# Kernel optimization log

Measured on AMD Instinct MI355X. Metric: run time of the kernel, lower is better.

## Reference

```python
import jax, jax.numpy as jnp
import numpy as np

B, T, D = 4, 2048, 2048
H, HD = 16, 128          # heads, head_dim (H*HD == D)
I = 5632                 # intermediate size
CAP = 0.25
K = int(T * CAP)         # 512 tokens selected per batch row
S = B * K                # packed sequence length
THETA = 10000.0
EPS = 1e-6


def setup_inputs() -> dict:
    key = jax.random.key(0)
    ks = jax.random.split(key, 12)
    s = 0.02
    w = lambda k, shp: jax.random.normal(k, shp, jnp.float32) * s
    return {
        "hidden_states": jax.random.normal(ks[0], (B, T, D), jnp.float32),
        "router_w": w(ks[1], (D,)),
        "router_b": jnp.zeros((1,), jnp.float32),
        "ln1_w": jnp.ones((D,), jnp.float32),
        "ln2_w": jnp.ones((D,), jnp.float32),
        "wq": w(ks[2], (D, D)), "bq": jnp.zeros((D,), jnp.float32),
        "wk": w(ks[3], (D, D)), "bk": jnp.zeros((D,), jnp.float32),
        "wv": w(ks[4], (D, D)), "bv": jnp.zeros((D,), jnp.float32),
        "wo": w(ks[5], (D, D)),
        "w_gate": w(ks[6], (D, I)),
        "w_up": w(ks[7], (D, I)),
        "w_down": w(ks[8], (I, D)),
    }


def _rms(x, w):
    return x * jax.lax.rsqrt(jnp.mean(x * x, axis=-1, keepdims=True) + EPS) * w


def _rotate_half(x):
    x1, x2 = jnp.split(x, 2, axis=-1)
    return jnp.concatenate([-x2, x1], axis=-1)


def reference(hidden_states, router_w, router_b, ln1_w, ln2_w,
              wq, bq, wk, bk, wv, bv, wo, w_gate, w_up, w_down):
    # ---- router: per-token scalar scores, top-k per batch row ----
    scores = hidden_states @ router_w + router_b[0]          # [B,T]
    _, idx = jax.lax.top_k(scores, K)                        # [B,K]
    idx = jnp.sort(idx, axis=-1)                             # causal order in packed seq

    # ---- gather selected tokens into packed batch-1 sequence ----
    sel = jnp.take_along_axis(hidden_states, idx[..., None], axis=1)  # [B,K,D]
    sel_scores = jnp.take_along_axis(scores, idx, axis=1)             # [B,K]
    x = sel.reshape(S, D)
    pos = idx.reshape(S)                                     # original token positions

    # ---- rotary tables gathered at original positions ----
    inv_freq = 1.0 / (THETA ** (jnp.arange(0, HD, 2, dtype=jnp.float32) / HD))
    freqs = pos.astype(jnp.float32)[:, None] * inv_freq[None, :]      # [S,HD/2]
    emb = jnp.concatenate([freqs, freqs], axis=-1)                    # [S,HD]
    cos, sin = jnp.cos(emb)[:, None, :], jnp.sin(emb)[:, None, :]     # [S,1,HD]

    # ---- Qwen2 decoder block (attention) ----
    h = _rms(x, ln1_w)
    q = (h @ wq + bq).reshape(S, H, HD)
    k = (h @ wk + bk).reshape(S, H, HD)
    v = (h @ wv + bv).reshape(S, H, HD)
    q = q * cos + _rotate_half(q) * sin
    k = k * cos + _rotate_half(k) * sin

    att = jnp.einsum("shd,thd->hst", q, k) / np.sqrt(HD).astype(np.float32)
    causal = jnp.tril(jnp.ones((S, S), bool))
    att = jnp.where(causal[None], att, jnp.finfo(att.dtype).min)
    p = jax.nn.softmax(att, axis=-1)
    attn_out = jnp.einsum("hst,thd->shd", p, v).reshape(S, D) @ wo
    x1 = x + attn_out

    # ---- Qwen2 decoder block (SwiGLU MLP) ----
    h2 = _rms(x1, ln2_w)
    mlp = (jax.nn.silu(h2 @ w_gate) * (h2 @ w_up)) @ w_down
    processed = x1 + mlp                                     # [S,D]

    # ---- sigmoid gate blend + scatter back ----
    gate = jax.nn.sigmoid(sel_scores).reshape(S, 1)
    blended = gate * processed + (1.0 - gate) * x            # [S,D]
    out = hidden_states.at[jnp.arange(B)[:, None], idx].set(blended.reshape(B, K, D))
    return out
```

## Files before the change

kernel.cpp:

```cpp
#include <hip/hip_runtime.h>
#include <stdint.h>

#define B_ 4
#define T_ 2048
#define D_ 2048
#define H_ 16
#define HD_ 128
#define I_ 5632
#define K_ 512
#define S_ 2048
#define D3_ (3 * D_)

typedef float f32x4 __attribute__((ext_vector_type(4)));
typedef short s16x8 __attribute__((ext_vector_type(8)));
typedef __bf16 bf16x8 __attribute__((ext_vector_type(8)));

template <typename V>
__device__ __forceinline__ auto mfma_try(V a, V b, f32x4 c, int)
    -> decltype(__builtin_amdgcn_mfma_f32_16x16x32_bf16(a, b, c, 0, 0, 0)) {
  return __builtin_amdgcn_mfma_f32_16x16x32_bf16(a, b, c, 0, 0, 0);
}
template <typename V>
__device__ __forceinline__ f32x4 mfma_try(V a, V b, f32x4 c, long) {
  return __builtin_amdgcn_mfma_f32_16x16x32_bf16(
      __builtin_bit_cast(bf16x8, a), __builtin_bit_cast(bf16x8, b), c, 0, 0, 0);
}
__device__ __forceinline__ f32x4 mfma_bf16(s16x8 a, s16x8 b, f32x4 c) {
  return mfma_try(a, b, c, 0);
}

__device__ __forceinline__ void gl_lds16(const void* g, void* l) {
  __builtin_amdgcn_global_load_lds((const __attribute__((address_space(1))) void*)g,
                                   (__attribute__((address_space(3))) void*)l, 16, 0, 0);
}

__device__ __forceinline__ unsigned short f2bf(float f) {
  unsigned u = __float_as_uint(f);
  u += 0x7FFFu + ((u >> 16) & 1);
  return (unsigned short)(u >> 16);
}
__device__ __forceinline__ float bf2f(unsigned short s) {
  return __uint_as_float(((unsigned)s) << 16);
}

__global__ __launch_bounds__(256) void k_copy_scores(const float4* __restrict__ hid,
                                                     float4* __restrict__ dst,
                                                     const float4* __restrict__ rw,
                                                     const float* __restrict__ rb,
                                                     float* __restrict__ scores) {
  int row = blockIdx.x, t = threadIdx.x;
  const float4* hr = hid + (size_t)row * (D_ / 4);
  float4* dr = dst + (size_t)row * (D_ / 4);
  float acc = 0.f;
#pragma unroll
  for (int i = 0; i < 2; i++) {
    float4 v = hr[t + i * 256];
    dr[t + i * 256] = v;
    float4 w = rw[t + i * 256];
    acc += v.x * w.x + v.y * w.y + v.z * w.z + v.w * w.w;
  }
#pragma unroll
  for (int d = 32; d; d >>= 1) acc += __shfl_xor(acc, d);
  __shared__ float red[4];
  if ((t & 63) == 0) red[t >> 6] = acc;
  __syncthreads();
  if (t == 0) scores[row] = red[0] + red[1] + red[2] + red[3] + rb[0];
}

__global__ __launch_bounds__(1024) void k_topk(const float* __restrict__ scores,
                                               int* __restrict__ pos) {
  __shared__ unsigned long long keys[T_];
  __shared__ int sidx[K_];
  int b = blockIdx.x, t = threadIdx.x;
  for (int i = t; i < T_; i += 1024) {
    unsigned u = __float_as_uint(scores[b * T_ + i]);
    u = (u & 0x80000000u) ? ~u : (u | 0x80000000u);
    keys[i] = ((unsigned long long)u << 32) | (unsigned)(~(unsigned)i);
  }
  __syncthreads();
  for (int k = 2; k <= T_; k <<= 1)
    for (int j = k >> 1; j > 0; j >>= 1) {
      for (int i = t; i < T_; i += 1024) {
        int l = i ^ j;
        if (l > i) {
          unsigned long long a = keys[i], c = keys[l];
          bool desc = ((i & k) == 0);
          if (desc ? (a < c) : (a > c)) { keys[i] = c; keys[l] = a; }
        }
      }
      __syncthreads();
    }
  if (t < K_) sidx[t] = (int)(~(unsigned)(keys[t] & 0xFFFFFFFFull));
  __syncthreads();
  for (int k = 2; k <= K_; k <<= 1)
    for (int j = k >> 1; j > 0; j >>= 1) {
      if (t < K_) {
        int i = t, l = i ^ j;
        if (l > i && l < K_) {
          int a = sidx[i], c = sidx[l];
          bool asc = ((i & k) == 0);
          if (asc ? (a > c) : (a < c)) { sidx[i] = c; sidx[l] = a; }
        }
      }
      __syncthreads();
    }
  if (t < K_) pos[b * K_ + t] = sidx[t];
}

__global__ __launch_bounds__(256) void k_gather(const float* __restrict__ hidden,
    const int* __restrict__ pos, const float* __restrict__ scores,
    const float* __restrict__ ln1w, float* __restrict__ x,
    unsigned short* __restrict__ xn, float* __restrict__ gate,
    float* __restrict__ cosb, float* __restrict__ sinb) {
  int s = blockIdx.x, t = threadIdx.x;
  int b = s >> 9, p = pos[s];
  const float* src = hidden + ((size_t)b * T_ + p) * D_;
  float v[8];
  float ss = 0.f;
#pragma unroll
  for (int i = 0; i < 8; i++) { v[i] = src[t + i * 256]; ss += v[i] * v[i]; }
  __shared__ float red[4];
#pragma unroll
  for (int d = 32; d; d >>= 1) ss += __shfl_xor(ss, d);
  if ((t & 63) == 0) red[t >> 6] = ss;
  __syncthreads();
  ss = red[0] + red[1] + red[2] + red[3];
  float scale = rsqrtf(ss / (float)D_ + 1e-6f);
  float* xd = x + (size_t)s * D_;
  unsigned short* xnd = xn + (size_t)s * D_;
#pragma unroll
  for (int i = 0; i < 8; i++) {
    int c = t + i * 256;
    xd[c] = v[i];
    xnd[c] = f2bf(v[i] * scale * ln1w[c]);
  }
  if (t == 0) gate[s] = 1.f / (1.f + expf(-scores[b * T_ + p]));
  if (t < 64) {
    float invf = powf(10000.0f, -(float)t / 64.0f);
    float f = (float)p * invf;
    cosb[s * 64 + t] = cosf(f);
    sinb[s * 64 + t] = sinf(f);
  }
}

__global__ __launch_bounds__(256) void k_transpose(const float* __restrict__ src,
                                                   unsigned short* __restrict__ dst,
                                                   int R, int C) {
  __shared__ float tile[32][33];
  int tx = threadIdx.x & 31, ty = threadIdx.x >> 5;
  int c0 = blockIdx.x * 32, r0 = blockIdx.y * 32;
#pragma unroll
  for (int i = 0; i < 4; i++) {
    int r = ty + i * 8;
    tile[r][tx] = src[(size_t)(r0 + r) * C + c0 + tx];
  }
  __syncthreads();
#pragma unroll
  for (int i = 0; i < 4; i++) {
    int r = ty + i * 8;
    dst[(size_t)(c0 + r) * R + r0 + tx] = f2bf(tile[tx][r]);
  }
}

#define SWZ(row) ((((row) >> 1) & 3) << 4)

__device__ __forceinline__ void stage16k(const unsigned short* __restrict__ g, int ldK,
                                         int row0, int k0, char* lds, int tid) {
#pragma unroll
  for (int c = 0; c < 2; c++) {
    int off = c * 8192 + tid * 16;
    int row = off >> 6;
    int cb = (off & 63) ^ SWZ(row);
    gl_lds16(g + (size_t)(row0 + row) * ldK + k0 + (cb >> 1), lds + off);
  }
}
__device__ __forceinline__ void stage8k(const unsigned short* __restrict__ g, int ldK,
                                        int row0, int k0, char* lds, int tid) {
  int off = tid * 16;
  int row = off >> 6;
  int cb = (off & 63) ^ SWZ(row);
  gl_lds16(g + (size_t)(row0 + row) * ldK + k0 + (cb >> 1), lds + off);
}
__device__ __forceinline__ void stage64r(const unsigned short* __restrict__ g, int ldK,
                                         int row0, int k0, char* lds, int tid) {
  int off = tid * 16;
  int row = off >> 6;
  int cb = (off & 63) ^ SWZ(row);
  gl_lds16(g + (size_t)(row0 + row) * ldK + k0 + (cb >> 1), lds + off);
}
__device__ __forceinline__ void stage128r(const unsigned short* __restrict__ g, int ldK,
                                          int row0, int k0, char* lds, int tid) {
#pragma unroll
  for (int c = 0; c < 2; c++) {
    int off = c * 4096 + tid * 16;
    int row = off >> 6;
    int cb = (off & 63) ^ SWZ(row);
    gl_lds16(g + (size_t)(row0 + row) * ldK + k0 + (cb >> 1), lds + off);
  }
}
__device__ __forceinline__ s16x8 ldfrag(const char* base, int row, int g) {
  return *(const s16x8*)(base + row * 64 + ((g * 16) ^ SWZ(row)));
}

__global__ __launch_bounds__(512, 2) void k_gemm_qkv8(const unsigned short* __restrict__ A,
    const unsigned short* __restrict__ Bt, unsigned short* __restrict__ C,
    const float* __restrict__ bq, const float* __restrict__ bk,
    const float* __restrict__ bv) {
  alignas(16) __shared__ short As[2][256 * 32];
  alignas(16) __shared__ short Bs[2][128 * 32];
  int tid = threadIdx.x;
  int lane = tid & 63, g = lane >> 4, lr = lane & 15;
  int wid = tid >> 6, wm = wid >> 1, wn = wid & 1;
  int m0 = blockIdx.x * 256, n0 = blockIdx.y * 128;
  f32x4 zero4 = {0.f, 0.f, 0.f, 0.f};
  f32x4 acc[4][4];
#pragma unroll
  for (int m = 0; m < 4; m++)
#pragma unroll
    for (int n = 0; n < 4; n++) acc[m][n] = zero4;
  const int nkt = D_ / 32;
  stage16k(A, D_, m0, 0, (char*)As[0], tid);
  stage8k(Bt, D_, n0, 0, (char*)Bs[0], tid);
  stage16k(A, D_, m0, 32, (char*)As[1], tid);
  stage8k(Bt, D_, n0, 32, (char*)Bs[1], tid);
  int arow = wm * 64 + lr;
  int brow = wn * 64 + lr;
  for (int t = 0; t < nkt; t++) {
    int b = t & 1;
    const char* Ab = (const char*)As[b];
    const char* Bb = (const char*)Bs[b];
    if (t + 1 < nkt) asm volatile("s_waitcnt vmcnt(3)" ::: "memory");
    else             asm volatile("s_waitcnt vmcnt(0)" ::: "memory");
    __builtin_amdgcn_s_barrier();
    s16x8 af[4], bf4[4];
#pragma unroll
    for (int i = 0; i < 4; i++) af[i] = ldfrag(Ab, arow + i * 16, g);
#pragma unroll
    for (int i = 0; i < 4; i++) bf4[i] = ldfrag(Bb, brow + i * 16, g);
    asm volatile("s_waitcnt lgkmcnt(0)" ::: "memory");
    __builtin_amdgcn_s_barrier();
    if (t + 2 < nkt) {
      stage16k(A, D_, m0, (t + 2) * 32, (char*)As[b], tid);
      stage8k(Bt, D_, n0, (t + 2) * 32, (char*)Bs[b], tid);
    }
    __builtin_amdgcn_s_setprio(1);
#pragma unroll
    for (int m = 0; m < 4; m++)
#pragma unroll
      for (int n = 0; n < 4; n++) acc[m][n] = mfma_bf16(af[m], bf4[n], acc[m][n]);
    __builtin_amdgcn_s_setprio(0);
  }
#pragma unroll
  for (int m = 0; m < 4; m++)
#pragma unroll
    for (int n = 0; n < 4; n++)
#pragma unroll
      for (int r = 0; r < 4; r++) {
        int row = m0 + wm * 64 + m * 16 + (g << 2) + r;
        int col = n0 + wn * 64 + n * 16 + lr;
        float bias = (col < D_) ? bq[col] : ((col < 2 * D_) ? bk[col - D_] : bv[col - 2 * D_]);
        C[(size_t)row * D3_ + col] = f2bf(acc[m][n][r] + bias);
      }
}

__global__ __launch_bounds__(512, 2) void k_gemm_gup8(const unsigned short* __restrict__ A,
    const unsigned short* __restrict__ Bg, const unsigned short* __restrict__ Bu,
    unsigned short* __restrict__ act) {
  alignas(16) __shared__ short As[2][256 * 32];
  alignas(16) __shared__ short Bgs[2][128 * 32];
  alignas(16) __shared__ short Bus[2][128 * 32];
  int tid = threadIdx.x;
  int lane = tid & 63, g = lane >> 4, lr = lane & 15;
  int wid = tid >> 6, wm = wid >> 1, wn = wid & 1;
  int m0 = blockIdx.x * 256, n0 = blockIdx.y * 128;
  f32x4 zero4 = {0.f, 0.f, 0.f, 0.f};
  f32x4 ag[4][4], au[4][4];
#pragma unroll
  for (int m = 0; m < 4; m++)
#pragma unroll
    for (int n = 0; n < 4; n++) { ag[m][n] = zero4; au[m][n] = zero4; }
  const int nkt = D_ / 32;
  stage16k(A, D_, m0, 0, (char*)As[0], tid);
  stage8k(Bg, D_, n0, 0, (char*)Bgs[0], tid);
  stage8k(Bu, D_, n0, 0, (char*)Bus[0], tid);
  stage16k(A, D_, m0, 32, (char*)As[1], tid);
  stage8k(Bg, D_, n0, 32, (char*)Bgs[1], tid);
  stage8k(Bu, D_, n0, 32, (char*)Bus[1], tid);
  int arow = wm * 64 + lr;
  int brow = wn * 64 + lr;
  for (int t = 0; t < nkt; t++) {
    int b = t & 1;
    const char* Ab = (const char*)As[b];
    const char* Bgb = (const char*)Bgs[b];
    const char* Bub = (const char*)Bus[b];
    if (t + 1 < nkt) asm volatile("s_waitcnt vmcnt(4)" ::: "memory");
    else             asm volatile("s_waitcnt vmcnt(0)" ::: "memory");
    __builtin_amdgcn_s_barrier();
    s16x8 af[4], bg4[4], bu4[4];
#pragma unroll
    for (int i = 0; i < 4; i++) af[i] = ldfrag(Ab, arow + i * 16, g);
#pragma unroll
    for (int i = 0; i < 4; i++) bg4[i] = ldfrag(Bgb, brow + i * 16, g);
#pragma unroll
    for (int i = 0; i < 4; i++) bu4[i] = ldfrag(Bub, brow + i * 16, g);
    asm volatile("s_waitcnt lgkmcnt(0)" ::: "memory");
    __builtin_amdgcn_s_barrier();
    if (t + 2 < nkt) {
      stage16k(A, D_, m0, (t + 2) * 32, (char*)As[b], tid);
      stage8k(Bg, D_, n0, (t + 2) * 32, (char*)Bgs[b], tid);
      stage8k(Bu, D_, n0, (t + 2) * 32, (char*)Bus[b], tid);
    }
    __builtin_amdgcn_s_setprio(1);
#pragma unroll
    for (int m = 0; m < 4; m++)
#pragma unroll
      for (int n = 0; n < 4; n++) {
        ag[m][n] = mfma_bf16(af[m], bg4[n], ag[m][n]);
        au[m][n] = mfma_bf16(af[m], bu4[n], au[m][n]);
      }
    __builtin_amdgcn_s_setprio(0);
  }
#pragma unroll
  for (int m = 0; m < 4; m++)
#pragma unroll
    for (int n = 0; n < 4; n++)
#pragma unroll
      for (int r = 0; r < 4; r++) {
        int row = m0 + wm * 64 + m * 16 + (g << 2) + r;
        int col = n0 + wn * 64 + n * 16 + lr;
        float gv = ag[m][n][r], uv = au[m][n][r];
        float si = gv / (1.f + __expf(-gv));
        act[(size_t)row * I_ + col] = f2bf(si * uv);
      }
}

__global__ __launch_bounds__(256, 2) void k_gemm_wo64(const unsigned short* __restrict__ A,
    const unsigned short* __restrict__ Bt, const float* __restrict__ xres,
    float* __restrict__ x1) {
  alignas(16) __shared__ short As[2][64 * 32];
  alignas(16) __shared__ short Bs[2][128 * 32];
  int tid = threadIdx.x;
  int lane = tid & 63, g = lane >> 4, lr = lane & 15, wid = tid >> 6;
  int m0 = blockIdx.x * 64, n0 = blockIdx.y * 128;
  f32x4 zero4 = {0.f, 0.f, 0.f, 0.f};
  f32x4 acc[4][2];
#pragma unroll
  for (int m = 0; m < 4; m++)
#pragma unroll
    for (int n = 0; n < 2; n++) acc[m][n] = zero4;
  const int nkt = D_ / 32;
  stage64r(A, D_, m0, 0, (char*)As[0], tid);
  stage128r(Bt, D_, n0, 0, (char*)Bs[0], tid);
  stage64r(A, D_, m0, 32, (char*)As[1], tid);
  stage128r(Bt, D_, n0, 32, (char*)Bs[1], tid);
  for (int t = 0; t < nkt; t++) {
    int b = t & 1;
    const char* Ab = (const char*)As[b];
    const char* Bb = (const char*)Bs[b];
    if (t + 1 < nkt) asm volatile("s_waitcnt vmcnt(3)" ::: "memory");
    else             asm volatile("s_waitcnt vmcnt(0)" ::: "memory");
    __builtin_amdgcn_s_barrier();
    s16x8 af[4], bf2[2];
#pragma unroll
    for (int i = 0; i < 4; i++) af[i] = ldfrag(Ab, i * 16 + lr, g);
#pragma unroll
    for (int j = 0; j < 2; j++) bf2[j] = ldfrag(Bb, wid * 32 + j * 16 + lr, g);
    asm volatile("s_waitcnt lgkmcnt(0)" ::: "memory");
    __builtin_amdgcn_s_barrier();
    if (t + 2 < nkt) {
      stage64r(A, D_, m0, (t + 2) * 32, (char*)As[b], tid);
      stage128r(Bt, D_, n0, (t + 2) * 32, (char*)Bs[b], tid);
    }
    __builtin_amdgcn_s_setprio(1);
#pragma unroll
    for (int m = 0; m < 4; m++)
#pragma unroll
      for (int n = 0; n < 2; n++) acc[m][n] = mfma_bf16(af[m], bf2[n], acc[m][n]);
    __builtin_amdgcn_s_setprio(0);
  }
#pragma unroll
  for (int m = 0; m < 4; m++)
#pragma unroll
    for (int n = 0; n < 2; n++)
#pragma unroll
      for (int r = 0; r < 4; r++) {
        int row = m0 + m * 16 + (g << 2) + r;
        int col = n0 + wid * 32 + n * 16 + lr;
        x1[(size_t)row * D_ + col] = acc[m][n][r] + xres[(size_t)row * D_ + col];
      }
}

__global__ __launch_bounds__(256, 2) void k_gemm_down64(const unsigned short* __restrict__ A,
    const unsigned short* __restrict__ Bt, const float* __restrict__ x1,
    const float* __restrict__ x, const float* __restrict__ gate,
    const int* __restrict__ pos, float* __restrict__ out) {
  alignas(16) __shared__ short As[2][64 * 32];
  alignas(16) __shared__ short Bs[2][128 * 32];
  int tid = threadIdx.x;
  int lane = tid & 63, g = lane >> 4, lr = lane & 15, wid = tid >> 6;
  int m0 = blockIdx.x * 64, n0 = blockIdx.y * 128;
  f32x4 zero4 = {0.f, 0.f, 0.f, 0.f};
  f32x4 acc[4][2];
#pragma unroll
  for (int m = 0; m < 4; m++)
#pragma unroll
    for (int n = 0; n < 2; n++) acc[m][n] = zero4;
  const int nkt = I_ / 32;
  stage64r(A, I_, m0, 0, (char*)As[0], tid);
  stage128r(Bt, I_, n0, 0, (char*)Bs[0], tid);
  stage64r(A, I_, m0, 32, (char*)As[1], tid);
  stage128r(Bt, I_, n0, 32, (char*)Bs[1], tid);
  for (int t = 0; t < nkt; t++) {
    int b = t & 1;
    const char* Ab = (const char*)As[b];
    const char* Bb = (const char*)Bs[b];
    if (t + 1 < nkt) asm volatile("s_waitcnt vmcnt(3)" ::: "memory");
    else             asm volatile("s_waitcnt vmcnt(0)" ::: "memory");
    __builtin_amdgcn_s_barrier();
    s16x8 af[4], bf2[2];
#pragma unroll
    for (int i = 0; i < 4; i++) af[i] = ldfrag(Ab, i * 16 + lr, g);
#pragma unroll
    for (int j = 0; j < 2; j++) bf2[j] = ldfrag(Bb, wid * 32 + j * 16 + lr, g);
    asm volatile("s_waitcnt lgkmcnt(0)" ::: "memory");
    __builtin_amdgcn_s_barrier();
    if (t + 2 < nkt) {
      stage64r(A, I_, m0, (t + 2) * 32, (char*)As[b], tid);
      stage128r(Bt, I_, n0, (t + 2) * 32, (char*)Bs[b], tid);
    }
    __builtin_amdgcn_s_setprio(1);
#pragma unroll
    for (int m = 0; m < 4; m++)
#pragma unroll
      for (int n = 0; n < 2; n++) acc[m][n] = mfma_bf16(af[m], bf2[n], acc[m][n]);
    __builtin_amdgcn_s_setprio(0);
  }
#pragma unroll
  for (int m = 0; m < 4; m++)
#pragma unroll
    for (int n = 0; n < 2; n++)
#pragma unroll
      for (int r = 0; r < 4; r++) {
        int srow = m0 + m * 16 + (g << 2) + r;
        int col = n0 + wid * 32 + n * 16 + lr;
        float proc = acc[m][n][r] + x1[(size_t)srow * D_ + col];
        float gt = gate[srow];
        float xv = x[(size_t)srow * D_ + col];
        int bb = srow >> 9;
        int p = pos[srow];
        out[((size_t)bb * T_ + p) * D_ + col] = gt * proc + (1.f - gt) * xv;
      }
}

__global__ __launch_bounds__(256) void k_rope(const unsigned short* __restrict__ qkv,
    const float* __restrict__ cosb, const float* __restrict__ sinb,
    unsigned short* __restrict__ qh, unsigned short* __restrict__ kh,
    unsigned short* __restrict__ vT) {
  int s0 = blockIdx.x * 64;
  int h = blockIdx.y;
  int t = threadIdx.x;
#pragma unroll
  for (int i = 0; i < 16; i++) {
    int flat = t + i * 256;
    int r = flat >> 6, dp = flat & 63;
    int s = s0 + r;
    float c = cosb[s * 64 + dp], sn = sinb[s * 64 + dp];
    const unsigned short* qrow = qkv + (size_t)s * D3_ + h * HD_;
    float q1 = bf2f(qrow[dp]), q2 = bf2f(qrow[dp + 64]);
    unsigned short* qdst = qh + ((size_t)h * S_ + s) * HD_;
    qdst[dp] = f2bf(q1 * c - q2 * sn);
    qdst[dp + 64] = f2bf(q2 * c + q1 * sn);
    const unsigned short* krow = qrow + D_;
    float k1 = bf2f(krow[dp]), k2 = bf2f(krow[dp + 64]);
    unsigned short* kdst = kh + ((size_t)h * S_ + s) * HD_;
    kdst[dp] = f2bf(k1 * c - k2 * sn);
    kdst[dp + 64] = f2bf(k2 * c + k1 * sn);
  }
  __shared__ unsigned short vt[128][66];
#pragma unroll
  for (int i = 0; i < 32; i++) {
    int flat = t + i * 256;
    int r = flat >> 7, d = flat & 127;
    vt[d][r] = qkv[(size_t)(s0 + r) * D3_ + 2 * D_ + h * HD_ + d];
  }
  __syncthreads();
#pragma unroll
  for (int i = 0; i < 32; i++) {
    int flat = t + i * 256;
    int d = flat >> 6, sc = flat & 63;
    vT[((size_t)h * HD_ + d) * S_ + s0 + sc] = vt[d][sc];
  }
}

__device__ __forceinline__ void stage_kv(const unsigned short* __restrict__ kh,
                                         const unsigned short* __restrict__ vT,
                                         size_t hbase, int kt, char* KsB, char* VsB, int tid) {
#pragma unroll
  for (int c = 0; c < 4; c++) {
    int off = c * 4096 + tid * 16;
    int row = off >> 8;
    int cb = (off & 255) ^ ((row & 7) << 4);
    gl_lds16(kh + hbase + (size_t)(kt * 64 + row) * HD_ + (cb >> 1), KsB + off);
  }
#pragma unroll
  for (int c = 0; c < 4; c++) {
    int off = c * 4096 + tid * 16;
    int row = off >> 7;
    int cb = (off & 127) ^ ((row & 7) << 4);
    gl_lds16(vT + hbase + (size_t)row * S_ + kt * 64 + (cb >> 1), VsB + off);
  }
}

__global__ __launch_bounds__(256, 2) void k_attn(const unsigned short* __restrict__ qh,
                                                 const unsigned short* __restrict__ kh,
                                                 const unsigned short* __restrict__ vT,
                                                 unsigned short* __restrict__ ao) {
  alignas(16) __shared__ short Ks[2][64 * 128];
  alignas(16) __shared__ short Vs[2][128 * 64];
  alignas(16) __shared__ short Ps[4][16 * 64];
  int bidx = blockIdx.x;
  int head = bidx & 15;
  int slot = bidx >> 4;
  int qt = (slot < 16) ? (31 - slot) : (slot - 16);
  int q0 = qt * 64;
  int tid = threadIdx.x, w = tid >> 6, lane = tid & 63, g = lane >> 4, lr = lane & 15;
  size_t hbase = (size_t)head * S_ * HD_;
  int qw = q0 + w * 16;
  char* PsW = (char*)&Ps[w][0];
  s16x8 qf[4];
#pragma unroll
  for (int ks = 0; ks < 4; ks++)
    qf[ks] = *(const s16x8*)&qh[hbase + (size_t)(qw + lr) * HD_ + ks * 32 + g * 8];
  f32x4 o[8];
  f32x4 zero4 = {0.f, 0.f, 0.f, 0.f};
#pragma unroll
  for (int nf = 0; nf < 8; nf++) o[nf] = zero4;
  float m_i[4], l_i[4];
#pragma unroll
  for (int r = 0; r < 4; r++) { m_i[r] = -1e30f; l_i[r] = 0.f; }
  const float sc = 0.08838834764831843f;

  stage_kv(kh, vT, hbase, 0, (char*)Ks[0], (char*)Vs[0], tid);
  if (qt > 0) stage_kv(kh, vT, hbase, 1, (char*)Ks[1], (char*)Vs[1], tid);

  for (int kt = 0; kt <= qt; kt++) {
    int b = kt & 1;
    const char* KsB = (const char*)Ks[b];
    const char* VsB = (const char*)Vs[b];
    if (kt < qt) asm volatile("s_waitcnt vmcnt(8)" ::: "memory");
    else         asm volatile("s_waitcnt vmcnt(0)" ::: "memory");
    __builtin_amdgcn_s_barrier();
    f32x4 sacc[4];
#pragma unroll
    for (int nf = 0; nf < 4; nf++) sacc[nf] = zero4;
#pragma unroll
    for (int ks = 0; ks < 4; ks++) {
      s16x8 kf[4];
#pragma unroll
      for (int nf = 0; nf < 4; nf++) {
        int row = nf * 16 + lr;
        kf[nf] = *(const s16x8*)(KsB + row * 256 + (((ks << 6) + (g << 4)) ^ ((row & 7) << 4)));
      }
#pragma unroll
      for (int nf = 0; nf < 4; nf++) sacc[nf] = mfma_bf16(qf[ks], kf[nf], sacc[nf]);
    }
    bool diag = (kt == qt);
#pragma unroll
    for (int r = 0; r < 4; r++) {
      int prow = (g << 2) + r;
      int qrow = qw + prow;
      float pv[4];
      float mx = -1e30f;
#pragma unroll
      for (int nf = 0; nf < 4; nf++) {
        float vv = sacc[nf][r] * sc;
        if (diag) {
          int kc = kt * 64 + nf * 16 + lr;
          vv = (kc <= qrow) ? vv : -1e30f;
        }
        pv[nf] = vv;
        mx = fmaxf(mx, vv);
      }
#pragma unroll
      for (int d = 1; d < 16; d <<= 1) mx = fmaxf(mx, __shfl_xor(mx, d));
      float mold = m_i[r], mnew = fmaxf(mold, mx);
      float corr = __expf(mold - mnew);
      float ssum = 0.f;
#pragma unroll
      for (int nf = 0; nf < 4; nf++) {
        float pe = __expf(pv[nf] - mnew);
        int cb = ((nf * 16 + lr) << 1) ^ ((prow & 7) << 4);
        *(unsigned short*)(PsW + prow * 128 + cb) = f2bf(pe);
        ssum += pe;
      }
#pragma unroll
      for (int d = 1; d < 16; d <<= 1) ssum += __shfl_xor(ssum, d);
      l_i[r] = l_i[r] * corr + ssum;
      m_i[r] = mnew;
#pragma unroll
      for (int nf = 0; nf < 8; nf++) o[nf][r] *= corr;
    }
    s16x8 pa[2];
#pragma unroll
    for (int ks = 0; ks < 2; ks++)
      pa[ks] = *(const s16x8*)(PsW + lr * 128 + (((ks << 6) + (g << 4)) ^ ((lr & 7) << 4)));
#pragma unroll
    for (int nf = 0; nf < 8; nf++) {
#pragma unroll
      for (int ks = 0; ks < 2; ks++) {
        int row = nf * 16 + lr;
        s16x8 vb = *(const s16x8*)(VsB + row * 128 + (((ks << 6) + (g << 4)) ^ ((row & 7) << 4)));
        o[nf] = mfma_bf16(pa[ks], vb, o[nf]);
      }
    }
    asm volatile("s_waitcnt lgkmcnt(0)" ::: "memory");
    __builtin_amdgcn_s_barrier();
    if (kt + 2 <= qt)
      stage_kv(kh, vT, hbase, kt + 2, (char*)Ks[b], (char*)Vs[b], tid);
  }
#pragma unroll
  for (int nf = 0; nf < 8; nf++)
#pragma unroll
    for (int r = 0; r < 4; r++) {
      int row = qw + (g << 2) + r;
      int col = head * HD_ + nf * 16 + lr;
      ao[(size_t)row * D_ + col] = f2bf(o[nf][r] / l_i[r]);
    }
}

__global__ __launch_bounds__(256) void k_rms2(const float* __restrict__ x1,
                                              const float* __restrict__ ln2w,
                                              unsigned short* __restrict__ xn2) {
  int s = blockIdx.x, t = threadIdx.x;
  const float* src = x1 + (size_t)s * D_;
  float v[8];
  float ss = 0.f;
#pragma unroll
  for (int i = 0; i < 8; i++) { v[i] = src[t + i * 256]; ss += v[i] * v[i]; }
  __shared__ float red[4];
#pragma unroll
  for (int d = 32; d; d >>= 1) ss += __shfl_xor(ss, d);
  if ((t & 63) == 0) red[t >> 6] = ss;
  __syncthreads();
  ss = red[0] + red[1] + red[2] + red[3];
  float scale = rsqrtf(ss / (float)D_ + 1e-6f);
  unsigned short* dst = xn2 + (size_t)s * D_;
#pragma unroll
  for (int i = 0; i < 8; i++) {
    int c = t + i * 256;
    dst[c] = f2bf(v[i] * scale * ln2w[c]);
  }
}

extern "C" void kernel_launch(void* const* d_in, const int* in_sizes, int n_in,
                              void* d_out, int out_size, void* d_ws, size_t ws_size,
                              hipStream_t stream) {
  (void)in_sizes; (void)n_in; (void)out_size; (void)ws_size;
  const float* hidden = (const float*)d_in[0];
  const float* router_w = (const float*)d_in[1];
  const float* router_b = (const float*)d_in[2];
  const float* ln1w = (const float*)d_in[3];
  const float* ln2w = (const float*)d_in[4];
  const float* wq = (const float*)d_in[5];
  const float* bq = (const float*)d_in[6];
  const float* wk = (const float*)d_in[7];
  const float* bk = (const float*)d_in[8];
  const float* wv = (const float*)d_in[9];
  const float* bv = (const float*)d_in[10];
  const float* wo = (const float*)d_in[11];
  const float* wg = (const float*)d_in[12];
  const float* wu = (const float*)d_in[13];
  const float* wd = (const float*)d_in[14];
  float* out = (float*)d_out;

  char* ws = (char*)d_ws;
  size_t off = 0;
  auto alloc = [&](size_t bytes) {
    char* p = ws + off;
    off += (bytes + 255) & ~(size_t)255;
    return p;
  };
  unsigned short* wqkvT = (unsigned short*)alloc(3ull * D_ * D_ * 2);
  unsigned short* woT = (unsigned short*)alloc((size_t)D_ * D_ * 2);
  unsigned short* wgT = (unsigned short*)alloc((size_t)I_ * D_ * 2);
  unsigned short* wuT = (unsigned short*)alloc((size_t)I_ * D_ * 2);
  unsigned short* wdT = (unsigned short*)alloc((size_t)D_ * I_ * 2);
  float* scores = (float*)alloc((size_t)B_ * T_ * 4);
  int* pos = (int*)alloc((size_t)S_ * 4);
  float* gate = (float*)alloc((size_t)S_ * 4);
  float* x = (float*)alloc((size_t)S_ * D_ * 4);
  float* x1 = (float*)alloc((size_t)S_ * D_ * 4);
  unsigned short* xn = (unsigned short*)alloc((size_t)S_ * D_ * 2);
  float* cosb = (float*)alloc((size_t)S_ * 64 * 4);
  float* sinb = (float*)alloc((size_t)S_ * 64 * 4);
  unsigned short* qkv = (unsigned short*)alloc((size_t)S_ * D3_ * 2);
  unsigned short* qh = (unsigned short*)alloc((size_t)H_ * S_ * HD_ * 2);
  unsigned short* kh = (unsigned short*)alloc((size_t)H_ * S_ * HD_ * 2);
  unsigned short* vT = (unsigned short*)alloc((size_t)H_ * S_ * HD_ * 2);
  unsigned short* ao = (unsigned short*)alloc((size_t)S_ * D_ * 2);

  k_copy_scores<<<B_ * T_, 256, 0, stream>>>((const float4*)hidden, (float4*)out,
                                             (const float4*)router_w, router_b, scores);

  k_transpose<<<dim3(D_ / 32, D_ / 32), 256, 0, stream>>>(wq, wqkvT, D_, D_);
  k_transpose<<<dim3(D_ / 32, D_ / 32), 256, 0, stream>>>(wk, wqkvT + (size_t)D_ * D_, D_, D_);
  k_transpose<<<dim3(D_ / 32, D_ / 32), 256, 0, stream>>>(wv, wqkvT + 2ull * D_ * D_, D_, D_);
  k_transpose<<<dim3(D_ / 32, D_ / 32), 256, 0, stream>>>(wo, woT, D_, D_);
  k_transpose<<<dim3(I_ / 32, D_ / 32), 256, 0, stream>>>(wg, wgT, D_, I_);
  k_transpose<<<dim3(I_ / 32, D_ / 32), 256, 0, stream>>>(wu, wuT, D_, I_);
  k_transpose<<<dim3(D_ / 32, I_ / 32), 256, 0, stream>>>(wd, wdT, I_, D_);

  k_topk<<<B_, 1024, 0, stream>>>(scores, pos);
  k_gather<<<S_, 256, 0, stream>>>(hidden, pos, scores, ln1w, x, xn, gate, cosb, sinb);

  k_gemm_qkv8<<<dim3(S_ / 256, D3_ / 128), 512, 0, stream>>>(xn, wqkvT, qkv, bq, bk, bv);
  k_rope<<<dim3(S_ / 64, H_), 256, 0, stream>>>(qkv, cosb, sinb, qh, kh, vT);
  k_attn<<<32 * H_, 256, 0, stream>>>(qh, kh, vT, ao);
  k_gemm_wo64<<<dim3(S_ / 64, D_ / 128), 256, 0, stream>>>(ao, woT, x, x1);
  k_rms2<<<S_, 256, 0, stream>>>(x1, ln2w, xn);
  k_gemm_gup8<<<dim3(S_ / 256, I_ / 128), 512, 0, stream>>>(xn, wgT, wuT, qkv);
  k_gemm_down64<<<dim3(S_ / 64, D_ / 128), 256, 0, stream>>>(qkv, wdT, x1, x, gate, pos, out);
}
```

Measured before the change: 566.9 us.

## Triple-buffer LDS in GEMM kernels to drop one barrier per k-step

Moves the QKV, Wo and down-projection GEMMs from double to triple LDS buffering. Each k-step now needs one barrier instead of two, and the LDS fragment reads overlap the prefetch issued for step t+2. The transpose kernel also writes four bf16 values per thread as a single vector store. The cost is 50% more shared memory per block, which may lower occupancy, notably for the 512-thread QKV kernel with launch bounds of 2 blocks.

Result: slower. 583.4 us (+2.9%).

```diff
diff --git a/kernel.cpp b/kernel.cpp
--- a/kernel.cpp
+++ b/kernel.cpp
@@ -155,11 +155,14 @@
     tile[r][tx] = src[(size_t)(r0 + r) * C + c0 + tx];
   }
   __syncthreads();
-#pragma unroll
-  for (int i = 0; i < 4; i++) {
-    int r = ty + i * 8;
-    dst[(size_t)(c0 + r) * R + r0 + tx] = f2bf(tile[tx][r]);
-  }
+  int drow = threadIdx.x >> 3;
+  int dc4 = (threadIdx.x & 7) * 4;
+  ushort4 v;
+  v.x = f2bf(tile[dc4 + 0][drow]);
+  v.y = f2bf(tile[dc4 + 1][drow]);
+  v.z = f2bf(tile[dc4 + 2][drow]);
+  v.w = f2bf(tile[dc4 + 3][drow]);
+  *(ushort4*)&dst[(size_t)(c0 + drow) * R + r0 + dc4] = v;
 }
 
 #define SWZ(row) ((((row) >> 1) & 3) << 4)
@@ -206,8 +209,8 @@
     const unsigned short* __restrict__ Bt, unsigned short* __restrict__ C,
     const float* __restrict__ bq, const float* __restrict__ bk,
     const float* __restrict__ bv) {
-  alignas(16) __shared__ short As[2][256 * 32];
-  alignas(16) __shared__ short Bs[2][128 * 32];
+  alignas(16) __shared__ short As[3 * 256 * 32];
+  alignas(16) __shared__ short Bs[3 * 128 * 32];
   int tid = threadIdx.x;
   int lane = tid & 63, g = lane >> 4, lr = lane & 15;
   int wid = tid >> 6, wm = wid >> 1, wn = wid & 1;
@@ -219,30 +222,29 @@
 #pragma unroll
     for (int n = 0; n < 4; n++) acc[m][n] = zero4;
   const int nkt = D_ / 32;
-  stage16k(A, D_, m0, 0, (char*)As[0], tid);
-  stage8k(Bt, D_, n0, 0, (char*)Bs[0], tid);
-  stage16k(A, D_, m0, 32, (char*)As[1], tid);
-  stage8k(Bt, D_, n0, 32, (char*)Bs[1], tid);
+  stage16k(A, D_, m0, 0, (char*)As, tid);
+  stage8k(Bt, D_, n0, 0, (char*)Bs, tid);
+  stage16k(A, D_, m0, 32, (char*)As + 16384, tid);
+  stage8k(Bt, D_, n0, 32, (char*)Bs + 8192, tid);
   int arow = wm * 64 + lr;
   int brow = wn * 64 + lr;
   for (int t = 0; t < nkt; t++) {
-    int b = t & 1;
-    const char* Ab = (const char*)As[b];
-    const char* Bb = (const char*)Bs[b];
-    if (t + 1 < nkt) asm volatile("s_waitcnt vmcnt(3)" ::: "memory");
-    else             asm volatile("s_waitcnt vmcnt(0)" ::: "memory");
-    __builtin_amdgcn_s_barrier();
-    s16x8 af[4], bf4[4];
-#pragma unroll
-    for (int i = 0; i < 4; i++) af[i] = ldfrag(Ab, arow + i * 16, g);
-#pragma unroll
-    for (int i = 0; i < 4; i++) bf4[i] = ldfrag(Bb, brow + i * 16, g);
-    asm volatile("s_waitcnt lgkmcnt(0)" ::: "memory");
+    int b = t % 3;
+    const char* Ab = (const char*)As + b * 16384;
+    const char* Bb = (const char*)Bs + b * 8192;
+    if (t + 1 < nkt) asm volatile("s_waitcnt vmcnt(3) lgkmcnt(0)" ::: "memory");
+    else             asm volatile("s_waitcnt vmcnt(0) lgkmcnt(0)" ::: "memory");
     __builtin_amdgcn_s_barrier();
     if (t + 2 < nkt) {
-      stage16k(A, D_, m0, (t + 2) * 32, (char*)As[b], tid);
-      stage8k(Bt, D_, n0, (t + 2) * 32, (char*)Bs[b], tid);
-    }
+      int nb = (t + 2) % 3;
+      stage16k(A, D_, m0, (t + 2) * 32, (char*)As + nb * 16384, tid);
+      stage8k(Bt, D_, n0, (t + 2) * 32, (char*)Bs + nb * 8192, tid);
+    }
+    s16x8 af[4], bf4[4];
+#pragma unroll
+    for (int i = 0; i < 4; i++) af[i] = ldfrag(Ab, arow + i * 16, g);
+#pragma unroll
+    for (int i = 0; i < 4; i++) bf4[i] = ldfrag(Bb, brow + i * 16, g);
     __builtin_amdgcn_s_setprio(1);
 #pragma unroll
     for (int m = 0; m < 4; m++)
@@ -337,8 +339,8 @@
 __global__ __launch_bounds__(256, 2) void k_gemm_wo64(const unsigned short* __restrict__ A,
     const unsigned short* __restrict__ Bt, const float* __restrict__ xres,
     float* __restrict__ x1) {
-  alignas(16) __shared__ short As[2][64 * 32];
-  alignas(16) __shared__ short Bs[2][128 * 32];
+  alignas(16) __shared__ short As[3 * 64 * 32];
+  alignas(16) __shared__ short Bs[3 * 128 * 32];
   int tid = threadIdx.x;
   int lane = tid & 63, g = lane >> 4, lr = lane & 15, wid = tid >> 6;
   int m0 = blockIdx.x * 64, n0 = blockIdx.y * 128;
@@ -349,28 +351,27 @@
 #pragma unroll
     for (int n = 0; n < 2; n++) acc[m][n] = zero4;
   const int nkt = D_ / 32;
-  stage64r(A, D_, m0, 0, (char*)As[0], tid);
-  stage128r(Bt, D_, n0, 0, (char*)Bs[0], tid);
-  stage64r(A, D_, m0, 32, (char*)As[1], tid);
-  stage128r(Bt, D_, n0, 32, (char*)Bs[1], tid);
+  stage64r(A, D_, m0, 0, (char*)As, tid);
+  stage128r(Bt, D_, n0, 0, (char*)Bs, tid);
+  stage64r(A, D_, m0, 32, (char*)As + 4096, tid);
+  stage128r(Bt, D_, n0, 32, (char*)Bs + 8192, tid);
   for (int t = 0; t < nkt; t++) {
-    int b = t & 1;
-    const char* Ab = (const char*)As[b];
-    const char* Bb = (const char*)Bs[b];
-    if (t + 1 < nkt) asm volatile("s_waitcnt vmcnt(3)" ::: "memory");
-    else             asm volatile("s_waitcnt vmcnt(0)" ::: "memory");
-    __builtin_amdgcn_s_barrier();
-    s16x8 af[4], bf2[2];
-#pragma unroll
-    for (int i = 0; i < 4; i++) af[i] = ldfrag(Ab, i * 16 + lr, g);
-#pragma unroll
-    for (int j = 0; j < 2; j++) bf2[j] = ldfrag(Bb, wid * 32 + j * 16 + lr, g);
-    asm volatile("s_waitcnt lgkmcnt(0)" ::: "memory");
+    int b = t % 3;
+    const char* Ab = (const char*)As + b * 4096;
+    const char* Bb = (const char*)Bs + b * 8192;
+    if (t + 1 < nkt) asm volatile("s_waitcnt vmcnt(3) lgkmcnt(0)" ::: "memory");
+    else             asm volatile("s_waitcnt vmcnt(0) lgkmcnt(0)" ::: "memory");
     __builtin_amdgcn_s_barrier();
     if (t + 2 < nkt) {
-      stage64r(A, D_, m0, (t + 2) * 32, (char*)As[b], tid);
-      stage128r(Bt, D_, n0, (t + 2) * 32, (char*)Bs[b], tid);
-    }
+      int nb = (t + 2) % 3;
+      stage64r(A, D_, m0, (t + 2) * 32, (char*)As + nb * 4096, tid);
+      stage128r(Bt, D_, n0, (t + 2) * 32, (char*)Bs + nb * 8192, tid);
+    }
+    s16x8 af[4], bf2[2];
+#pragma unroll
+    for (int i = 0; i < 4; i++) af[i] = ldfrag(Ab, i * 16 + lr, g);
+#pragma unroll
+    for (int j = 0; j < 2; j++) bf2[j] = ldfrag(Bb, wid * 32 + j * 16 + lr, g);
     __builtin_amdgcn_s_setprio(1);
 #pragma unroll
     for (int m = 0; m < 4; m++)
@@ -394,8 +395,8 @@
     const unsigned short* __restrict__ Bt, const float* __restrict__ x1,
     const float* __restrict__ x, const float* __restrict__ gate,
     const int* __restrict__ pos, float* __restrict__ out) {
-  alignas(16) __shared__ short As[2][64 * 32];
-  alignas(16) __shared__ short Bs[2][128 * 32];
+  alignas(16) __shared__ short As[3 * 64 * 32];
+  alignas(16) __shared__ short Bs[3 * 128 * 32];
   int tid = threadIdx.x;
   int lane = tid & 63, g = lane >> 4, lr = lane & 15, wid = tid >> 6;
   int m0 = blockIdx.x * 64, n0 = blockIdx.y * 128;
@@ -406,28 +407,27 @@
 #pragma unroll
     for (int n = 0; n < 2; n++) acc[m][n] = zero4;
   const int nkt = I_ / 32;
-  stage64r(A, I_, m0, 0, (char*)As[0], tid);
-  stage128r(Bt, I_, n0, 0, (char*)Bs[0], tid);
-  stage64r(A, I_, m0, 32, (char*)As[1], tid);
-  stage128r(Bt, I_, n0, 32, (char*)Bs[1], tid);
+  stage64r(A, I_, m0, 0, (char*)As, tid);
+  stage128r(Bt, I_, n0, 0, (char*)Bs, tid);
+  stage64r(A, I_, m0, 32, (char*)As + 4096, tid);
+  stage128r(Bt, I_, n0, 32, (char*)Bs + 8192, tid);
   for (int t = 0; t < nkt; t++) {
-    int b = t & 1;
-    const char* Ab = (const char*)As[b];
-    const char* Bb = (const char*)Bs[b];
-    if (t + 1 < nkt) asm volatile("s_waitcnt vmcnt(3)" ::: "memory");
-    else             asm volatile("s_waitcnt vmcnt(0)" ::: "memory");
-    __builtin_amdgcn_s_barrier();
-    s16x8 af[4], bf2[2];
-#pragma unroll
-    for (int i = 0; i < 4; i++) af[i] = ldfrag(Ab, i * 16 + lr, g);
-#pragma unroll
-    for (int j = 0; j < 2; j++) bf2[j] = ldfrag(Bb, wid * 32 + j * 16 + lr, g);
-    asm volatile("s_waitcnt lgkmcnt(0)" ::: "memory");
+    int b = t % 3;
+    const char* Ab = (const char*)As + b * 4096;
+    const char* Bb = (const char*)Bs + b * 8192;
+    if (t + 1 < nkt) asm volatile("s_waitcnt vmcnt(3) lgkmcnt(0)" ::: "memory");
+    else             asm volatile("s_waitcnt vmcnt(0) lgkmcnt(0)" ::: "memory");
     __builtin_amdgcn_s_barrier();
     if (t + 2 < nkt) {
-      stage64r(A, I_, m0, (t + 2) * 32, (char*)As[b], tid);
-      stage128r(Bt, I_, n0, (t + 2) * 32, (char*)Bs[b], tid);
-    }
+      int nb = (t + 2) % 3;
+      stage64r(A, I_, m0, (t + 2) * 32, (char*)As + nb * 4096, tid);
+      stage128r(Bt, I_, n0, (t + 2) * 32, (char*)Bs + nb * 8192, tid);
+    }
+    s16x8 af[4], bf2[2];
+#pragma unroll
+    for (int i = 0; i < 4; i++) af[i] = ldfrag(Ab, i * 16 + lr, g);
+#pragma unroll
+    for (int j = 0; j < 2; j++) bf2[j] = ldfrag(Bb, wid * 32 + j * 16 + lr, g);
     __builtin_amdgcn_s_setprio(1);
 #pragma unroll
     for (int m = 0; m < 4; m++)
```

## Restructure gate/up GEMM into a 128-wide K pipeline with fine-grained staging

Applied to the files above, without the earlier changes.

Replaces the gate/up SwiGLU GEMM with a version that stages 64-element K tiles into a 128KB double-buffered LDS region using an XOR swizzle. Staging is split into quarter-tile chunks interleaved between separate MFMA phases for the gate and up accumulators, so global loads overlap with compute at finer granularity. Occupancy drops to one block per CU. The weight transpose kernel also switches to vectorized 4-element bf16 stores.

New measurement: 537.5 us. 1.05x faster.

```diff
diff --git a/kernel.cpp b/kernel.cpp
--- a/kernel.cpp
+++ b/kernel.cpp
@@ -155,11 +155,14 @@
     tile[r][tx] = src[(size_t)(r0 + r) * C + c0 + tx];
   }
   __syncthreads();
-#pragma unroll
-  for (int i = 0; i < 4; i++) {
-    int r = ty + i * 8;
-    dst[(size_t)(c0 + r) * R + r0 + tx] = f2bf(tile[tx][r]);
-  }
+  int drow = threadIdx.x >> 3;
+  int dc4 = (threadIdx.x & 7) * 4;
+  ushort4 v;
+  v.x = f2bf(tile[dc4 + 0][drow]);
+  v.y = f2bf(tile[dc4 + 1][drow]);
+  v.z = f2bf(tile[dc4 + 2][drow]);
+  v.w = f2bf(tile[dc4 + 3][drow]);
+  *(ushort4*)&dst[(size_t)(c0 + drow) * R + r0 + dc4] = v;
 }
 
 #define SWZ(row) ((((row) >> 1) & 3) << 4)
@@ -263,12 +266,35 @@
       }
 }
 
-__global__ __launch_bounds__(512, 2) void k_gemm_gup8(const unsigned short* __restrict__ A,
+__device__ __forceinline__ void stage_u(const unsigned short* __restrict__ g, int ldK,
+                                        int grow0, int k0, char* ldsbase, int tid) {
+#pragma unroll
+  for (int c = 0; c < 2; c++) {
+    int off = c * 8192 + tid * 16;
+    int row = off >> 7;
+    int cb = (off & 127) ^ ((row & 7) << 4);
+    gl_lds16(g + (size_t)(grow0 + row) * ldK + k0 + (cb >> 1), ldsbase + off);
+  }
+}
+__device__ __forceinline__ s16x8 ldfrag128(const char* base, int row, int byteoff) {
+  return *(const s16x8*)(base + row * 128 + (byteoff ^ ((row & 7) << 4)));
+}
+
+#define GUP_MFMA(AF, BB, ACC)                                       \
+  __builtin_amdgcn_s_barrier();                                     \
+  asm volatile("s_waitcnt lgkmcnt(0)" ::: "memory");                \
+  __builtin_amdgcn_sched_barrier(0);                                \
+  __builtin_amdgcn_s_setprio(1);                                    \
+  _Pragma("unroll") for (int m = 0; m < 4; m++)                     \
+    _Pragma("unroll") for (int n = 0; n < 4; n++)                   \
+      ACC[m][n] = mfma_bf16(AF[m], BB[n], ACC[m][n]);               \
+  __builtin_amdgcn_s_setprio(0);                                    \
+  __builtin_amdgcn_s_barrier();
+
+__global__ __launch_bounds__(512, 1) void k_gemm_gup8p(const unsigned short* __restrict__ A,
     const unsigned short* __restrict__ Bg, const unsigned short* __restrict__ Bu,
     unsigned short* __restrict__ act) {
-  alignas(16) __shared__ short As[2][256 * 32];
-  alignas(16) __shared__ short Bgs[2][128 * 32];
-  alignas(16) __shared__ short Bus[2][128 * 32];
+  alignas(16) __shared__ char L[2][65536];
   int tid = threadIdx.x;
   int lane = tid & 63, g = lane >> 4, lr = lane & 15;
   int wid = tid >> 6, wm = wid >> 1, wn = wid & 1;
@@ -279,46 +305,72 @@
   for (int m = 0; m < 4; m++)
 #pragma unroll
     for (int n = 0; n < 4; n++) { ag[m][n] = zero4; au[m][n] = zero4; }
-  const int nkt = D_ / 32;
-  stage16k(A, D_, m0, 0, (char*)As[0], tid);
-  stage8k(Bg, D_, n0, 0, (char*)Bgs[0], tid);
-  stage8k(Bu, D_, n0, 0, (char*)Bus[0], tid);
-  stage16k(A, D_, m0, 32, (char*)As[1], tid);
-  stage8k(Bg, D_, n0, 32, (char*)Bgs[1], tid);
-  stage8k(Bu, D_, n0, 32, (char*)Bus[1], tid);
   int arow = wm * 64 + lr;
   int brow = wn * 64 + lr;
-  for (int t = 0; t < nkt; t++) {
-    int b = t & 1;
-    const char* Ab = (const char*)As[b];
-    const char* Bgb = (const char*)Bgs[b];
-    const char* Bub = (const char*)Bus[b];
-    if (t + 1 < nkt) asm volatile("s_waitcnt vmcnt(4)" ::: "memory");
-    else             asm volatile("s_waitcnt vmcnt(0)" ::: "memory");
-    __builtin_amdgcn_s_barrier();
-    s16x8 af[4], bg4[4], bu4[4];
-#pragma unroll
-    for (int i = 0; i < 4; i++) af[i] = ldfrag(Ab, arow + i * 16, g);
-#pragma unroll
-    for (int i = 0; i < 4; i++) bg4[i] = ldfrag(Bgb, brow + i * 16, g);
-#pragma unroll
-    for (int i = 0; i < 4; i++) bu4[i] = ldfrag(Bub, brow + i * 16, g);
-    asm volatile("s_waitcnt lgkmcnt(0)" ::: "memory");
-    __builtin_amdgcn_s_barrier();
-    if (t + 2 < nkt) {
-      stage16k(A, D_, m0, (t + 2) * 32, (char*)As[b], tid);
-      stage8k(Bg, D_, n0, (t + 2) * 32, (char*)Bgs[b], tid);
-      stage8k(Bu, D_, n0, (t + 2) * 32, (char*)Bus[b], tid);
-    }
-    __builtin_amdgcn_s_setprio(1);
-#pragma unroll
-    for (int m = 0; m < 4; m++)
-#pragma unroll
-      for (int n = 0; n < 4; n++) {
-        ag[m][n] = mfma_bf16(af[m], bg4[n], ag[m][n]);
-        au[m][n] = mfma_bf16(af[m], bu4[n], au[m][n]);
-      }
-    __builtin_amdgcn_s_setprio(0);
+  const int NI = D_ / 128;
+  stage_u(A, D_, m0, 0, &L[0][0], tid);
+  stage_u(A, D_, m0 + 128, 0, &L[0][16384], tid);
+  stage_u(Bg, D_, n0, 0, &L[0][32768], tid);
+  stage_u(Bu, D_, n0, 0, &L[0][49152], tid);
+  stage_u(A, D_, m0, 64, &L[1][0], tid);
+  asm volatile("s_waitcnt vmcnt(2)" ::: "memory");
+  __builtin_amdgcn_s_barrier();
+  for (int i = 0; i < NI; i++) {
+    const char* B0 = &L[0][0];
+    const char* B1 = &L[1][0];
+    int k1 = i * 128 + 64;
+    int k2 = i * 128 + 128;
+    int k3 = i * 128 + 192;
+    bool more = (i + 1 < NI);
+    s16x8 af0[4], af1[4], bb[4];
+#pragma unroll
+    for (int q = 0; q < 4; q++) af0[q] = ldfrag128(B0, arow + q * 16, g * 16);
+#pragma unroll
+    for (int q = 0; q < 4; q++) bb[q] = ldfrag128(B0 + 32768, brow + q * 16, g * 16);
+    stage_u(A, D_, m0 + 128, k1, &L[1][16384], tid);
+    asm volatile("s_waitcnt vmcnt(4)" ::: "memory");
+    GUP_MFMA(af0, bb, ag);
+#pragma unroll
+    for (int q = 0; q < 4; q++) bb[q] = ldfrag128(B0 + 49152, brow + q * 16, g * 16);
+    stage_u(Bg, D_, n0, k1, &L[1][32768], tid);
+    GUP_MFMA(af0, bb, au);
+#pragma unroll
+    for (int q = 0; q < 4; q++) af1[q] = ldfrag128(B0, arow + q * 16, 64 + g * 16);
+#pragma unroll
+    for (int q = 0; q < 4; q++) bb[q] = ldfrag128(B0 + 32768, brow + q * 16, 64 + g * 16);
+    stage_u(Bu, D_, n0, k1, &L[1][49152], tid);
+    GUP_MFMA(af1, bb, ag);
+#pragma unroll
+    for (int q = 0; q < 4; q++) bb[q] = ldfrag128(B0 + 49152, brow + q * 16, 64 + g * 16);
+    if (more) {
+      stage_u(A, D_, m0, k2, &L[0][0], tid);
+      asm volatile("s_waitcnt vmcnt(4)" ::: "memory");
+    } else {
+      asm volatile("s_waitcnt vmcnt(0)" ::: "memory");
+    }
+    GUP_MFMA(af1, bb, au);
+#pragma unroll
+    for (int q = 0; q < 4; q++) af0[q] = ldfrag128(B1, arow + q * 16, g * 16);
+#pragma unroll
+    for (int q = 0; q < 4; q++) bb[q] = ldfrag128(B1 + 32768, brow + q * 16, g * 16);
+    if (more) stage_u(A, D_, m0 + 128, k2, &L[0][16384], tid);
+    asm volatile("s_waitcnt vmcnt(4)" ::: "memory");
+    GUP_MFMA(af0, bb, ag);
+#pragma unroll
+    for (int q = 0; q < 4; q++) bb[q] = ldfrag128(B1 + 49152, brow + q * 16, g * 16);
+    if (more) stage_u(Bg, D_, n0, k2, &L[0][32768], tid);
+    GUP_MFMA(af0, bb, au);
+#pragma unroll
+    for (int q = 0; q < 4; q++) af1[q] = ldfrag128(B1, arow + q * 16, 64 + g * 16);
+#pragma unroll
+    for (int q = 0; q < 4; q++) bb[q] = ldfrag128(B1 + 32768, brow + q * 16, 64 + g * 16);
+    if (more) stage_u(Bu, D_, n0, k2, &L[0][49152], tid);
+    GUP_MFMA(af1, bb, ag);
+#pragma unroll
+    for (int q = 0; q < 4; q++) bb[q] = ldfrag128(B1 + 49152, brow + q * 16, 64 + g * 16);
+    if (more) stage_u(A, D_, m0, k3, &L[1][0], tid);
+    asm volatile("s_waitcnt vmcnt(4)" ::: "memory");
+    GUP_MFMA(af1, bb, au);
   }
 #pragma unroll
   for (int m = 0; m < 4; m++)
@@ -718,6 +770,6 @@
   k_attn<<<32 * H_, 256, 0, stream>>>(qh, kh, vT, ao);
   k_gemm_wo64<<<dim3(S_ / 64, D_ / 128), 256, 0, stream>>>(ao, woT, x, x1);
   k_rms2<<<S_, 256, 0, stream>>>(x1, ln2w, xn);
-  k_gemm_gup8<<<dim3(S_ / 256, I_ / 128), 512, 0, stream>>>(xn, wgT, wuT, qkv);
+  k_gemm_gup8p<<<dim3(S_ / 256, I_ / 128), 512, 0, stream>>>(xn, wgT, wuT, qkv);
   k_gemm_down64<<<dim3(S_ / 64, D_ / 128), 256, 0, stream>>>(qkv, wdT, x1, x, gate, pos, out);
 }
```
